# Optimization experiments

Measured on AMD Instinct MI355X. Metric: run time of the kernel, lower is better.

Reference implementation:

```python
import jax, jax.numpy as jnp
import numpy as np

B, D_IN, H, V, T = 8192, 2048, 1024, 6, 6  # batch, enc input, hidden, total_vocab, max_length
TAU = 1.0

def setup_inputs() -> dict:
    key = jax.random.key(0)
    ks = jax.random.split(key, 16)
    s = 0.02
    return {
        "x": jax.random.normal(ks[0], (B, D_IN), jnp.float32),
        "u_noise": jax.random.uniform(ks[1], (T, B, V), jnp.float32),
        "W_enc": jax.random.normal(ks[2], (D_IN, H), jnp.float32) * s,
        "b_enc": jnp.zeros((H,), jnp.float32),
        "start_embed": jax.random.normal(ks[3], (H,), jnp.float32) * 0.01,
        "W_tok": jax.random.normal(ks[4], (V, H), jnp.float32) * s,
        "b_tok": jnp.zeros((H,), jnp.float32),
        "Wz": jax.random.normal(ks[5], (2 * H, H), jnp.float32) * s,
        "bz": jnp.zeros((H,), jnp.float32),
        "Wr": jax.random.normal(ks[6], (2 * H, H), jnp.float32) * s,
        "br": jnp.zeros((H,), jnp.float32),
        "Wh": jax.random.normal(ks[7], (2 * H, H), jnp.float32) * s,
        "bh": jnp.zeros((H,), jnp.float32),
        "W_out": jax.random.normal(ks[8], (H, V), jnp.float32) * s,
        "b_out": jnp.zeros((V,), jnp.float32),
    }

def reference(x, u_noise, W_enc, b_enc, start_embed, W_tok, b_tok,
              Wz, bz, Wr, br, Wh, bh, W_out, b_out):
    eps = 1e-10
    # uniform -> Gumbel(0,1) noise, precomputed per step: (T, B, V)
    g_all = -jnp.log(-jnp.log(u_noise + eps) + eps)
    h0 = x @ W_enc + b_enc                                   # encoder: (B, H)
    batch = x.shape[0]
    prev0 = jnp.broadcast_to(start_embed, (batch, start_embed.shape[0]))
    rc0 = jnp.ones((batch, 1), x.dtype)                      # running continue mask
    nt0 = jnp.zeros((batch,), x.dtype)                       # differentiable token count

    def step(carry, g):
        h, prev, rc, nt = carry
        nt = nt + rc[:, 0]
        comb = jnp.concatenate([prev, h], axis=-1)           # (B, 2H)
        z = jax.nn.sigmoid(comb @ Wz + bz)
        r = jax.nn.sigmoid(comb @ Wr + br)
        comb_r = jnp.concatenate([prev, r * h], axis=-1)
        h_tilde = jnp.tanh(comb_r @ Wh + bh)
        h = (1 - z) * h + z * h_tilde                        # GRU update
        logits = h @ W_out + b_out                           # (B, V)
        # hard gumbel-softmax with straight-through estimator
        y_soft = jax.nn.softmax((logits + g) / TAU, axis=-1)
        y_hard = jax.nn.one_hot(jnp.argmax(y_soft, axis=-1), logits.shape[-1],
                                dtype=logits.dtype)
        token = y_hard - jax.lax.stop_gradient(y_soft) + y_soft
        masked = token * rc                                  # zero out after STOP
        rc = rc * (1 - token[:, -1:])                        # STOP is last symbol
        prev = token @ W_tok + b_tok
        return (h, prev, rc, nt), (masked, logits)

    (_, _, _, n_tokens), (masked_seq, logits_seq) = jax.lax.scan(
        step, (h0, prev0, rc0, nt0), g_all)
    # (T, B, V) -> (B, T*V) message
    message = jnp.transpose(masked_seq, (1, 0, 2)).reshape(batch, -1)
    return message, logits_seq, n_tokens
```

## Files before the change

kernel.cpp:

```cpp
#include <hip/hip_runtime.h>
#include <math.h>

#define B_ 8192
#define DIN_ 2048
#define H_ 1024
#define V_ 6
#define T_ 6

typedef short bf16x8 __attribute__((ext_vector_type(8)));
typedef float f32x4 __attribute__((ext_vector_type(4)));

__device__ __forceinline__ unsigned short f32_bf16(float f) {
    unsigned u = __float_as_uint(f);
    u += 0x7FFFu + ((u >> 16) & 1u);
    return (unsigned short)(u >> 16);
}
__device__ __forceinline__ float bf16_f32(unsigned short h) {
    return __uint_as_float(((unsigned)h) << 16);
}

#define GLL16(g, l) __builtin_amdgcn_global_load_lds(                       \
        (const __attribute__((address_space(1))) void*)(g),                  \
        (__attribute__((address_space(3))) void*)(l), 16, 0, 0)

__global__ __launch_bounds__(256) void conv_w(const float* __restrict__ W,
        unsigned short* __restrict__ hi, unsigned short* __restrict__ lo)
{
    const int t = blockIdx.x * 256 + threadIdx.x;
    const int n = t & 1023;
    const int kb = t >> 10;
    unsigned hq[4], lq[4];
#pragma unroll
    for (int p = 0; p < 4; ++p) {
        const float v0 = W[(size_t)(kb * 8 + 2 * p) * 1024 + n];
        const float v1 = W[(size_t)(kb * 8 + 2 * p + 1) * 1024 + n];
        const unsigned short h0 = f32_bf16(v0), h1 = f32_bf16(v1);
        const unsigned short l0 = f32_bf16(v0 - bf16_f32(h0));
        const unsigned short l1 = f32_bf16(v1 - bf16_f32(h1));
        hq[p] = (unsigned)h0 | ((unsigned)h1 << 16);
        lq[p] = (unsigned)l0 | ((unsigned)l1 << 16);
    }
    const size_t c = ((size_t)(n >> 4) * 256 + kb) * 128 + (size_t)(n & 15) * 8;
    *(uint4*)(hi + c) = make_uint4(hq[0], hq[1], hq[2], hq[3]);
    *(uint4*)(lo + c) = make_uint4(lq[0], lq[1], lq[2], lq[3]);
}

__global__ __launch_bounds__(256) void conv_wb(const float* __restrict__ W,
        unsigned short* __restrict__ hi, unsigned short* __restrict__ lo)
{
    const int t = blockIdx.x * 256 + threadIdx.x;
    const int n = t & 1023;
    const int kb = t >> 10;
    unsigned hq[4], lq[4];
#pragma unroll
    for (int p = 0; p < 4; ++p) {
        const float v0 = W[(size_t)(1024 + kb * 8 + 2 * p) * 1024 + n];
        const float v1 = W[(size_t)(1024 + kb * 8 + 2 * p + 1) * 1024 + n];
        const unsigned short h0 = f32_bf16(v0), h1 = f32_bf16(v1);
        const unsigned short l0 = f32_bf16(v0 - bf16_f32(h0));
        const unsigned short l1 = f32_bf16(v1 - bf16_f32(h1));
        hq[p] = (unsigned)h0 | ((unsigned)h1 << 16);
        lq[p] = (unsigned)l0 | ((unsigned)l1 << 16);
    }
    const size_t c = ((size_t)(n >> 4) * 128 + kb) * 128 + (size_t)(n & 15) * 8;
    *(uint4*)(hi + c) = make_uint4(hq[0], hq[1], hq[2], hq[3]);
    *(uint4*)(lo + c) = make_uint4(lq[0], lq[1], lq[2], lq[3]);
}

__global__ __launch_bounds__(256) void conv_x(const float* __restrict__ X,
        unsigned short* __restrict__ hi, unsigned short* __restrict__ lo)
{
    const size_t t = (size_t)blockIdx.x * 256 + threadIdx.x;
    const int kb = (int)(t & 255);
    const int m = (int)(t >> 8);
    const float4 f0 = *(const float4*)(X + (size_t)m * 2048 + kb * 8);
    const float4 f1 = *(const float4*)(X + (size_t)m * 2048 + kb * 8 + 4);
    const float v[8] = {f0.x, f0.y, f0.z, f0.w, f1.x, f1.y, f1.z, f1.w};
    unsigned hq[4], lq[4];
#pragma unroll
    for (int p = 0; p < 4; ++p) {
        const unsigned short h0 = f32_bf16(v[2 * p]);
        const unsigned short h1 = f32_bf16(v[2 * p + 1]);
        const unsigned short l0 = f32_bf16(v[2 * p] - bf16_f32(h0));
        const unsigned short l1 = f32_bf16(v[2 * p + 1] - bf16_f32(h1));
        hq[p] = (unsigned)h0 | ((unsigned)h1 << 16);
        lq[p] = (unsigned)l0 | ((unsigned)l1 << 16);
    }
    const size_t c = ((size_t)(m >> 4) * 256 + kb) * 128 + (size_t)(m & 15) * 8;
    *(uint4*)(hi + c) = make_uint4(hq[0], hq[1], hq[2], hq[3]);
    *(uint4*)(lo + c) = make_uint4(lq[0], lq[1], lq[2], lq[3]);
}

__global__ __launch_bounds__(256) void prep_tables(
        const float* __restrict__ Wz, const float* __restrict__ Wr,
        const float* __restrict__ Wh,
        const float* __restrict__ bz, const float* __restrict__ br,
        const float* __restrict__ bh,
        const float* __restrict__ Wt, const float* __restrict__ bt,
        const float* __restrict__ se,
        float* __restrict__ Pz, float* __restrict__ Pr, float* __restrict__ Ph)
{
    __shared__ float emb[7][1024];
    const int tid = threadIdx.x;
    for (int i = tid; i < 7 * 1024; i += 256) {
        const int r = i >> 10, k = i & 1023;
        emb[r][k] = (r < 6) ? (Wt[(size_t)r * 1024 + k] + bt[k]) : se[k];
    }
    __syncthreads();
    const float* W = (blockIdx.y == 0) ? Wz : ((blockIdx.y == 1) ? Wr : Wh);
    const float* bb = (blockIdx.y == 0) ? bz : ((blockIdx.y == 1) ? br : bh);
    float* P = (blockIdx.y == 0) ? Pz : ((blockIdx.y == 1) ? Pr : Ph);
    const int n = blockIdx.x * 256 + tid;
    float acc[7] = {0.f, 0.f, 0.f, 0.f, 0.f, 0.f, 0.f};
    for (int k = 0; k < 1024; ++k) {
        const float wv = W[(size_t)k * 1024 + n];
#pragma unroll
        for (int r = 0; r < 7; ++r) acc[r] = fmaf(emb[r][k], wv, acc[r]);
    }
    const float bvv = bb[n];
#pragma unroll
    for (int r = 0; r < 7; ++r) P[(size_t)r * 1024 + n] = acc[r] + bvv;
}

__global__ __launch_bounds__(256) void init_misc(
        int* __restrict__ tokidx, float* __restrict__ rc, float* __restrict__ nt)
{
    const int t = blockIdx.x * 256 + threadIdx.x;
    tokidx[t] = 6;
    rc[t] = 1.0f;
    nt[t] = 0.0f;
}

__global__ __launch_bounds__(256, 3)
void gemm_bt(
    const unsigned short* __restrict__ A_hi, const unsigned short* __restrict__ A_lo,
    const unsigned short* __restrict__ B0_hi, const unsigned short* __restrict__ B0_lo,
    const unsigned short* __restrict__ B1_hi, const unsigned short* __restrict__ B1_lo,
    const float* __restrict__ P0, const float* __restrict__ P1,
    const int* __restrict__ tokidx,
    const float* __restrict__ zbuf, float* __restrict__ hbuf,
    float* __restrict__ outf,
    unsigned short* __restrict__ ophi, unsigned short* __restrict__ oplo,
    int nkb, int mode)
{
    __shared__ unsigned short lds[16384];

    const int tid = threadIdx.x;
    const int lane = tid & 63;
    const int w = tid >> 6;

    const int NX = gridDim.x;
    const int lin = blockIdx.y * NX + blockIdx.x;
    const int xcd = lin & 7;
    const int idx = lin >> 3;
    int bx = idx % NX;
    const int by = xcd * 8 + idx / NX;

    const unsigned short* Bhi = B0_hi;
    const unsigned short* Blo = B0_lo;
    const float* Pm = P0;
    int isR = 0;
    if (mode == 1 && bx >= 8) { bx -= 8; Bhi = B1_hi; Blo = B1_lo; Pm = P1; isR = 1; }

    const int m0 = by * 128;
    const int n0 = bx * 128;
    const int gma0 = by * 8 + 2 * w;
    const int gnb0 = bx * 8 + 2 * w;

    unsigned short* dA0h = lds + (2 * w) * 512 + lane * 8;
    unsigned short* dA1h = lds + (2 * w + 1) * 512 + lane * 8;
    unsigned short* dA0l = lds + 4096 + (2 * w) * 512 + lane * 8;
    unsigned short* dA1l = lds + 4096 + (2 * w + 1) * 512 + lane * 8;
    unsigned short* dB0h = lds + 8192 + (2 * w) * 512 + lane * 8;
    unsigned short* dB1h = lds + 8192 + (2 * w + 1) * 512 + lane * 8;
    unsigned short* dB0l = lds + 12288 + (2 * w) * 512 + lane * 8;
    unsigned short* dB1l = lds + 12288 + (2 * w + 1) * 512 + lane * 8;

    f32x4 acc[4][4];
#pragma unroll
    for (int i = 0; i < 4; ++i)
#pragma unroll
        for (int j = 0; j < 4; ++j) acc[i][j] = (f32x4){0.f, 0.f, 0.f, 0.f};

    const int wr = w >> 1, wc = w & 1;
    const int fq = lane >> 4;
    const int fm = lane & 15;
    const int nsteps = nkb >> 2;

#pragma unroll 1
    for (int s = 0; s < nsteps; ++s) {
        __syncthreads();
        const size_t o0 = ((size_t)gma0 * nkb + s * 4) * 128 + lane * 8;
        const size_t o1 = o0 + (size_t)nkb * 128;
        GLL16(A_hi + o0, dA0h); GLL16(A_lo + o0, dA0l);
        GLL16(A_hi + o1, dA1h); GLL16(A_lo + o1, dA1l);
        const size_t b0 = ((size_t)gnb0 * nkb + s * 4) * 128 + lane * 8;
        const size_t b1 = b0 + (size_t)nkb * 128;
        GLL16(Bhi + b0, dB0h); GLL16(Blo + b0, dB0l);
        GLL16(Bhi + b1, dB1h); GLL16(Blo + b1, dB1l);
        __syncthreads();

        bf16x8 ah[4], al[4], bh4[4], bl4[4];
#pragma unroll
        for (int i = 0; i < 4; ++i) {
            const int ra = (wr * 4 + i) * 512 + fq * 128 + fm * 8;
            ah[i] = *(const bf16x8*)(lds + ra);
            al[i] = *(const bf16x8*)(lds + 4096 + ra);
            const int rb = (wc * 4 + i) * 512 + fq * 128 + fm * 8;
            bh4[i] = *(const bf16x8*)(lds + 8192 + rb);
            bl4[i] = *(const bf16x8*)(lds + 12288 + rb);
        }
#pragma unroll
        for (int i = 0; i < 4; ++i)
#pragma unroll
            for (int j = 0; j < 4; ++j) {
                acc[i][j] = __builtin_amdgcn_mfma_f32_16x16x32_bf16(ah[i], bh4[j], acc[i][j], 0, 0, 0);
                acc[i][j] = __builtin_amdgcn_mfma_f32_16x16x32_bf16(ah[i], bl4[j], acc[i][j], 0, 0, 0);
                acc[i][j] = __builtin_amdgcn_mfma_f32_16x16x32_bf16(al[i], bh4[j], acc[i][j], 0, 0, 0);
            }
    }

#pragma unroll
    for (int i = 0; i < 4; ++i) {
        int toks[4];
#pragma unroll
        for (int r = 0; r < 4; ++r) {
            const int row = m0 + wr * 64 + i * 16 + fq * 4 + r;
            toks[r] = tokidx ? tokidx[row] : 0;
        }
#pragma unroll
        for (int j = 0; j < 4; ++j) {
            const int col = n0 + wc * 64 + j * 16 + fm;
#pragma unroll
            for (int r = 0; r < 4; ++r) {
                const int row = m0 + wr * 64 + i * 16 + fq * 4 + r;
                const float v = acc[i][j][r] + Pm[(size_t)toks[r] * 1024 + col];
                const size_t off = (size_t)row * 1024 + col;
                const size_t pc = ((size_t)(row >> 4) * 128 + (col >> 3)) * 128
                                  + (size_t)(row & 15) * 8 + (col & 7);
                if (mode == 0) {
                    hbuf[off] = v;
                    const unsigned short hv = f32_bf16(v);
                    ophi[pc] = hv;
                    oplo[pc] = f32_bf16(v - bf16_f32(hv));
                } else if (mode == 1) {
                    const float sg = 1.0f / (1.0f + expf(-v));
                    if (!isR) {
                        outf[off] = sg;
                    } else {
                        const float rh = sg * hbuf[off];
                        const unsigned short hv = f32_bf16(rh);
                        ophi[pc] = hv;
                        oplo[pc] = f32_bf16(rh - bf16_f32(hv));
                    }
                } else {
                    const float tv = tanhf(v);
                    const float zv = zbuf[off];
                    const float hn = (1.0f - zv) * hbuf[off] + zv * tv;
                    hbuf[off] = hn;
                    const unsigned short hv = f32_bf16(hn);
                    ophi[pc] = hv;
                    oplo[pc] = f32_bf16(hn - bf16_f32(hv));
                }
            }
        }
    }
}

__global__ __launch_bounds__(256)
void step_tok(const float* __restrict__ h,
              const float* __restrict__ W_out, const float* __restrict__ b_out,
              const float* __restrict__ u,
              float* __restrict__ rc, float* __restrict__ nt,
              int* __restrict__ tokidx,
              float* __restrict__ out_msg, float* __restrict__ out_logits,
              float* __restrict__ out_nt, int t)
{
    const int lane = threadIdx.x & 63;
    const int wv = threadIdx.x >> 6;
    const int b = blockIdx.x * 4 + wv;

    const float* hr = h + (size_t)b * H_;
    float s[6] = {0.f, 0.f, 0.f, 0.f, 0.f, 0.f};
#pragma unroll
    for (int i = 0; i < 4; ++i) {
        const int k0 = i * 256 + lane * 4;
        const float4 hv = *(const float4*)(hr + k0);
        const float he[4] = {hv.x, hv.y, hv.z, hv.w};
#pragma unroll
        for (int e = 0; e < 4; ++e) {
            const float* wp = W_out + (size_t)(k0 + e) * V_;
            const float xv = he[e];
#pragma unroll
            for (int v = 0; v < 6; ++v) s[v] = fmaf(xv, wp[v], s[v]);
        }
    }
#pragma unroll
    for (int m = 1; m < 64; m <<= 1) {
#pragma unroll
        for (int v = 0; v < 6; ++v) s[v] += __shfl_xor(s[v], m, 64);
    }

    float lg[6];
#pragma unroll
    for (int v = 0; v < 6; ++v) lg[v] = s[v] + b_out[v];

    const float* ub = u + (size_t)b * V_;
    const float eps = 1e-10f;
    float aa[6];
#pragma unroll
    for (int v = 0; v < 6; ++v) {
        const float g = -logf(-logf(ub[v] + eps) + eps);
        aa[v] = lg[v] + g;
    }
    int tok = 0;
    float best = aa[0];
#pragma unroll
    for (int v = 1; v < 6; ++v)
        if (aa[v] > best) { best = aa[v]; tok = v; }

    if (lane == 0) {
        const float rco = rc[b];
#pragma unroll
        for (int v = 0; v < 6; ++v) out_logits[(size_t)b * 6 + v] = lg[v];
#pragma unroll
        for (int v = 0; v < 6; ++v)
            out_msg[(size_t)b * 36 + t * 6 + v] = (v == tok) ? rco : 0.0f;
        const float ntn = nt[b] + rco;
        nt[b] = ntn;
        out_nt[b] = ntn;
        rc[b] = (tok == 5) ? 0.0f : rco;
        tokidx[b] = tok;
    }
}

extern "C" void kernel_launch(void* const* d_in, const int* in_sizes, int n_in,
                              void* d_out, int out_size, void* d_ws, size_t ws_size,
                              hipStream_t stream)
{
    (void)in_sizes; (void)n_in; (void)out_size; (void)ws_size;
    const float* x       = (const float*)d_in[0];
    const float* u_noise = (const float*)d_in[1];
    const float* W_enc   = (const float*)d_in[2];
    const float* b_enc   = (const float*)d_in[3];
    const float* start_e = (const float*)d_in[4];
    const float* W_tok   = (const float*)d_in[5];
    const float* b_tok   = (const float*)d_in[6];
    const float* Wz      = (const float*)d_in[7];
    const float* bz      = (const float*)d_in[8];
    const float* Wr      = (const float*)d_in[9];
    const float* br      = (const float*)d_in[10];
    const float* Wh      = (const float*)d_in[11];
    const float* bh      = (const float*)d_in[12];
    const float* W_out   = (const float*)d_in[13];
    const float* b_out   = (const float*)d_in[14];

    float* out = (float*)d_out;
    float* out_msg = out;
    float* out_logits = out + (size_t)B_ * T_ * V_;
    float* out_nt = out_logits + (size_t)T_ * B_ * V_;

    char* wsb = (char*)d_ws;
    const size_t MB = 1024 * 1024;
    unsigned short* wzb_hi = (unsigned short*)(wsb + 0 * MB);
    unsigned short* wzb_lo = (unsigned short*)(wsb + 2 * MB);
    unsigned short* wrb_hi = (unsigned short*)(wsb + 4 * MB);
    unsigned short* wrb_lo = (unsigned short*)(wsb + 6 * MB);
    unsigned short* whb_hi = (unsigned short*)(wsb + 8 * MB);
    unsigned short* whb_lo = (unsigned short*)(wsb + 10 * MB);
    unsigned short* we_hi  = (unsigned short*)(wsb + 12 * MB);
    unsigned short* we_lo  = (unsigned short*)(wsb + 16 * MB);
    unsigned short* x_hi   = (unsigned short*)(wsb + 20 * MB);
    unsigned short* x_lo   = (unsigned short*)(wsb + 52 * MB);
    float*  zbuf  = (float*)(wsb + 20 * MB);
    unsigned short* rh_hi  = (unsigned short*)(wsb + 52 * MB);
    unsigned short* rh_lo  = (unsigned short*)(wsb + 68 * MB);
    float*  hbuf  = (float*)(wsb + 84 * MB);
    unsigned short* h_hi   = (unsigned short*)(wsb + 116 * MB);
    unsigned short* h_lo   = (unsigned short*)(wsb + 132 * MB);
    float* Pz = (float*)(wsb + 148 * MB);
    float* Pr = Pz + 7 * 1024;
    float* Ph = Pr + 7 * 1024;
    int* tokidx = (int*)(Ph + 7 * 1024);
    float* rcb = (float*)(tokidx + B_);
    float* ntb = rcb + B_;

    conv_wb<<<512, 256, 0, stream>>>(Wz, wzb_hi, wzb_lo);
    conv_wb<<<512, 256, 0, stream>>>(Wr, wrb_hi, wrb_lo);
    conv_wb<<<512, 256, 0, stream>>>(Wh, whb_hi, whb_lo);
    conv_w<<<1024, 256, 0, stream>>>(W_enc, we_hi, we_lo);
    conv_x<<<8192, 256, 0, stream>>>(x, x_hi, x_lo);
    prep_tables<<<dim3(4, 3), 256, 0, stream>>>(Wz, Wr, Wh, bz, br, bh,
                                                W_tok, b_tok, start_e, Pz, Pr, Ph);
    init_misc<<<32, 256, 0, stream>>>(tokidx, rcb, ntb);

    gemm_bt<<<dim3(8, 64), 256, 0, stream>>>(
        x_hi, x_lo, we_hi, we_lo, nullptr, nullptr,
        b_enc, nullptr, nullptr,
        nullptr, hbuf, nullptr, h_hi, h_lo, 256, 0);

    for (int t = 0; t < T_; ++t) {
        gemm_bt<<<dim3(16, 64), 256, 0, stream>>>(
            h_hi, h_lo, wzb_hi, wzb_lo, wrb_hi, wrb_lo,
            Pz, Pr, tokidx,
            nullptr, hbuf, zbuf, rh_hi, rh_lo, 128, 1);
        gemm_bt<<<dim3(8, 64), 256, 0, stream>>>(
            rh_hi, rh_lo, whb_hi, whb_lo, nullptr, nullptr,
            Ph, nullptr, tokidx,
            zbuf, hbuf, nullptr, h_hi, h_lo, 128, 2);
        step_tok<<<B_ / 4, 256, 0, stream>>>(
            hbuf, W_out, b_out, u_noise + (size_t)t * B_ * V_,
            rcb, ntb, tokidx, out_msg,
            out_logits + (size_t)t * B_ * V_, out_nt, t);
    }
}
```

Measured before the change: 1.746 ms.

## Rewrite GEMM as 256x128 tile, 512 threads, triple-buffered LDS pipeline

Widens the GEMM block to 512 threads covering 256 rows by 128 columns and splits the hi/lo loading across wave halves. Adds a three-stage LDS ring buffer with direct global-to-LDS prefetch two steps ahead, explicit vmcnt waits, raw barriers and MFMA priority hints. This is meant to hide global load latency behind MFMA work and raise reuse of B tiles. In exchange it uses much more LDS per block (144KB), which lowers occupancy, and the hand-tuned waitcnt counts could be wrong.

New measurement: 1.876 ms. 1.07x slower.

```diff
diff --git a/kernel.cpp b/kernel.cpp
--- a/kernel.cpp
+++ b/kernel.cpp
@@ -131,8 +131,8 @@
     nt[t] = 0.0f;
 }
 
-__global__ __launch_bounds__(256, 3)
-void gemm_bt(
+__global__ __launch_bounds__(512, 2)
+void gemm256(
     const unsigned short* __restrict__ A_hi, const unsigned short* __restrict__ A_lo,
     const unsigned short* __restrict__ B0_hi, const unsigned short* __restrict__ B0_lo,
     const unsigned short* __restrict__ B1_hi, const unsigned short* __restrict__ B1_lo,
@@ -143,7 +143,7 @@
     unsigned short* __restrict__ ophi, unsigned short* __restrict__ oplo,
     int nkb, int mode)
 {
-    __shared__ unsigned short lds[16384];
+    __shared__ unsigned short lds[3 * 24576];
 
     const int tid = threadIdx.x;
     const int lane = tid & 63;
@@ -154,7 +154,7 @@
     const int xcd = lin & 7;
     const int idx = lin >> 3;
     int bx = idx % NX;
-    const int by = xcd * 8 + idx / NX;
+    const int by = xcd * 4 + idx / NX;
 
     const unsigned short* Bhi = B0_hi;
     const unsigned short* Blo = B0_lo;
@@ -162,19 +162,16 @@
     int isR = 0;
     if (mode == 1 && bx >= 8) { bx -= 8; Bhi = B1_hi; Blo = B1_lo; Pm = P1; isR = 1; }
 
-    const int m0 = by * 128;
+    const int m0 = by * 256;
     const int n0 = bx * 128;
-    const int gma0 = by * 8 + 2 * w;
-    const int gnb0 = bx * 8 + 2 * w;
-
-    unsigned short* dA0h = lds + (2 * w) * 512 + lane * 8;
-    unsigned short* dA1h = lds + (2 * w + 1) * 512 + lane * 8;
-    unsigned short* dA0l = lds + 4096 + (2 * w) * 512 + lane * 8;
-    unsigned short* dA1l = lds + 4096 + (2 * w + 1) * 512 + lane * 8;
-    unsigned short* dB0h = lds + 8192 + (2 * w) * 512 + lane * 8;
-    unsigned short* dB1h = lds + 8192 + (2 * w + 1) * 512 + lane * 8;
-    unsigned short* dB0l = lds + 12288 + (2 * w) * 512 + lane * 8;
-    unsigned short* dB1l = lds + 12288 + (2 * w + 1) * 512 + lane * 8;
+    const int mg0 = by * 16;
+    const int ng0 = bx * 8;
+
+    const int pa = w >> 2;
+    const int ga0 = (w & 3) * 4;
+    const int nb0 = (w & 3) * 2;
+    const unsigned short* Asrc = pa ? A_lo : A_hi;
+    const unsigned short* Bsrc = pa ? Blo : Bhi;
 
     f32x4 acc[4][4];
 #pragma unroll
@@ -182,43 +179,84 @@
 #pragma unroll
         for (int j = 0; j < 4; ++j) acc[i][j] = (f32x4){0.f, 0.f, 0.f, 0.f};
 
-    const int wr = w >> 1, wc = w & 1;
+    const int wr = w & 3;
+    const int wc = w >> 2;
     const int fq = lane >> 4;
     const int fm = lane & 15;
     const int nsteps = nkb >> 2;
 
+#define STAGE(tt, bb) do {                                                     \
+    unsigned short* db_ = lds + (bb) * 24576;                                  \
+    const size_t kb0_ = (size_t)(tt) * 4;                                      \
+    _Pragma("unroll")                                                          \
+    for (int q = 0; q < 4; ++q) {                                              \
+        const size_t so = ((size_t)(mg0 + ga0 + q) * nkb + kb0_) * 128 + lane * 8; \
+        GLL16(Asrc + so, db_ + pa * 8192 + (ga0 + q) * 512 + lane * 8);        \
+    }                                                                          \
+    _Pragma("unroll")                                                          \
+    for (int q = 0; q < 2; ++q) {                                              \
+        const size_t so = ((size_t)(ng0 + nb0 + q) * nkb + kb0_) * 128 + lane * 8; \
+        GLL16(Bsrc + so, db_ + 16384 + pa * 4096 + (nb0 + q) * 512 + lane * 8);\
+    }                                                                          \
+} while (0)
+
+#define COMPUTE(bb) do {                                                       \
+    const unsigned short* db_ = lds + (bb) * 24576;                            \
+    bf16x8 bh4_[4], bl4_[4];                                                   \
+    _Pragma("unroll")                                                          \
+    for (int j = 0; j < 4; ++j) {                                              \
+        const int rb = 16384 + (wc * 4 + j) * 512 + fq * 128 + fm * 8;         \
+        bh4_[j] = *(const bf16x8*)(db_ + rb);                                  \
+        bl4_[j] = *(const bf16x8*)(db_ + rb + 4096);                           \
+    }                                                                          \
+    _Pragma("unroll")                                                          \
+    for (int i = 0; i < 4; ++i) {                                              \
+        const int ra = (wr * 4 + i) * 512 + fq * 128 + fm * 8;                 \
+        const bf16x8 ah = *(const bf16x8*)(db_ + ra);                          \
+        const bf16x8 al = *(const bf16x8*)(db_ + ra + 8192);                   \
+        __builtin_amdgcn_s_setprio(1);                                         \
+        _Pragma("unroll")                                                      \
+        for (int j = 0; j < 4; ++j) {                                          \
+            acc[i][j] = __builtin_amdgcn_mfma_f32_16x16x32_bf16(ah, bh4_[j], acc[i][j], 0, 0, 0); \
+            acc[i][j] = __builtin_amdgcn_mfma_f32_16x16x32_bf16(ah, bl4_[j], acc[i][j], 0, 0, 0); \
+            acc[i][j] = __builtin_amdgcn_mfma_f32_16x16x32_bf16(al, bh4_[j], acc[i][j], 0, 0, 0); \
+        }                                                                      \
+        __builtin_amdgcn_s_setprio(0);                                         \
+    }                                                                          \
+} while (0)
+
+    STAGE(0, 0);
+    STAGE(1, 1);
+
+    int cb = 0;
 #pragma unroll 1
-    for (int s = 0; s < nsteps; ++s) {
-        __syncthreads();
-        const size_t o0 = ((size_t)gma0 * nkb + s * 4) * 128 + lane * 8;
-        const size_t o1 = o0 + (size_t)nkb * 128;
-        GLL16(A_hi + o0, dA0h); GLL16(A_lo + o0, dA0l);
-        GLL16(A_hi + o1, dA1h); GLL16(A_lo + o1, dA1l);
-        const size_t b0 = ((size_t)gnb0 * nkb + s * 4) * 128 + lane * 8;
-        const size_t b1 = b0 + (size_t)nkb * 128;
-        GLL16(Bhi + b0, dB0h); GLL16(Blo + b0, dB0l);
-        GLL16(Bhi + b1, dB1h); GLL16(Blo + b1, dB1l);
-        __syncthreads();
-
-        bf16x8 ah[4], al[4], bh4[4], bl4[4];
-#pragma unroll
-        for (int i = 0; i < 4; ++i) {
-            const int ra = (wr * 4 + i) * 512 + fq * 128 + fm * 8;
-            ah[i] = *(const bf16x8*)(lds + ra);
-            al[i] = *(const bf16x8*)(lds + 4096 + ra);
-            const int rb = (wc * 4 + i) * 512 + fq * 128 + fm * 8;
-            bh4[i] = *(const bf16x8*)(lds + 8192 + rb);
-            bl4[i] = *(const bf16x8*)(lds + 12288 + rb);
-        }
-#pragma unroll
-        for (int i = 0; i < 4; ++i)
-#pragma unroll
-            for (int j = 0; j < 4; ++j) {
-                acc[i][j] = __builtin_amdgcn_mfma_f32_16x16x32_bf16(ah[i], bh4[j], acc[i][j], 0, 0, 0);
-                acc[i][j] = __builtin_amdgcn_mfma_f32_16x16x32_bf16(ah[i], bl4[j], acc[i][j], 0, 0, 0);
-                acc[i][j] = __builtin_amdgcn_mfma_f32_16x16x32_bf16(al[i], bh4[j], acc[i][j], 0, 0, 0);
-            }
-    }
+    for (int t = 0; t < nsteps - 2; ++t) {
+        const int sb = (cb >= 1) ? (cb - 1) : 2;
+        STAGE(t + 2, sb);
+        asm volatile("s_waitcnt vmcnt(12)" ::: "memory");
+        __builtin_amdgcn_s_barrier();
+        __builtin_amdgcn_sched_barrier(0);
+        COMPUTE(cb);
+        asm volatile("s_waitcnt lgkmcnt(0)" ::: "memory");
+        __builtin_amdgcn_s_barrier();
+        __builtin_amdgcn_sched_barrier(0);
+        cb = (cb == 2) ? 0 : cb + 1;
+    }
+    asm volatile("s_waitcnt vmcnt(6)" ::: "memory");
+    __builtin_amdgcn_s_barrier();
+    __builtin_amdgcn_sched_barrier(0);
+    COMPUTE(cb);
+    asm volatile("s_waitcnt lgkmcnt(0)" ::: "memory");
+    __builtin_amdgcn_s_barrier();
+    __builtin_amdgcn_sched_barrier(0);
+    cb = (cb == 2) ? 0 : cb + 1;
+    asm volatile("s_waitcnt vmcnt(0)" ::: "memory");
+    __builtin_amdgcn_s_barrier();
+    __builtin_amdgcn_sched_barrier(0);
+    COMPUTE(cb);
+
+#undef STAGE
+#undef COMPUTE
 
 #pragma unroll
     for (int i = 0; i < 4; ++i) {
@@ -394,17 +432,17 @@
                                                 W_tok, b_tok, start_e, Pz, Pr, Ph);
     init_misc<<<32, 256, 0, stream>>>(tokidx, rcb, ntb);
 
-    gemm_bt<<<dim3(8, 64), 256, 0, stream>>>(
+    gemm256<<<dim3(8, 32), 512, 0, stream>>>(
         x_hi, x_lo, we_hi, we_lo, nullptr, nullptr,
         b_enc, nullptr, nullptr,
         nullptr, hbuf, nullptr, h_hi, h_lo, 256, 0);
 
     for (int t = 0; t < T_; ++t) {
-        gemm_bt<<<dim3(16, 64), 256, 0, stream>>>(
+        gemm256<<<dim3(16, 32), 512, 0, stream>>>(
             h_hi, h_lo, wzb_hi, wzb_lo, wrb_hi, wrb_lo,
             Pz, Pr, tokidx,
             nullptr, hbuf, zbuf, rh_hi, rh_lo, 128, 1);
-        gemm_bt<<<dim3(8, 64), 256, 0, stream>>>(
+        gemm256<<<dim3(8, 32), 512, 0, stream>>>(
             rh_hi, rh_lo, whb_hi, whb_lo, nullptr, nullptr,
             Ph, nullptr, tokidx,
             zbuf, hbuf, nullptr, h_hi, h_lo, 128, 2);
```

## Fuse z and r gate GEMMs into one kernel sharing the A tile

Applied to the files above, without the earlier changes.

Adds a gemm_zr kernel that computes the z and r gate products together for the same 128x128 output tile. Each block loads the h tile once and reuses it against both Wz and Wr, so A traffic is halved and the grid goes from 16x64 to 8x64 blocks. The cost is two accumulator sets per thread, which raises register pressure (launch bounds ask for 2 blocks per CU), and a larger LDS footprint.

Result: slower. 1.904 ms (+9.0%).

```diff
diff --git a/kernel.cpp b/kernel.cpp
--- a/kernel.cpp
+++ b/kernel.cpp
@@ -267,6 +267,133 @@
     }
 }
 
+__global__ __launch_bounds__(256, 2)
+void gemm_zr(
+    const unsigned short* __restrict__ A_hi, const unsigned short* __restrict__ A_lo,
+    const unsigned short* __restrict__ Bz_hi, const unsigned short* __restrict__ Bz_lo,
+    const unsigned short* __restrict__ Br_hi, const unsigned short* __restrict__ Br_lo,
+    const float* __restrict__ Pz, const float* __restrict__ Pr,
+    const int* __restrict__ tokidx,
+    const float* __restrict__ hbuf, float* __restrict__ zbuf,
+    unsigned short* __restrict__ ophi, unsigned short* __restrict__ oplo,
+    int nkb)
+{
+    __shared__ unsigned short lds[24576];
+
+    const int tid = threadIdx.x;
+    const int lane = tid & 63;
+    const int w = tid >> 6;
+
+    const int NX = gridDim.x;
+    const int lin = blockIdx.y * NX + blockIdx.x;
+    const int xcd = lin & 7;
+    const int idx = lin >> 3;
+    const int bx = idx % NX;
+    const int by = xcd * 8 + idx / NX;
+
+    const int m0 = by * 128;
+    const int n0 = bx * 128;
+    const int gma0 = by * 8 + 2 * w;
+    const int gnb0 = bx * 8 + 2 * w;
+
+    unsigned short* dAh0 = lds +         (2 * w) * 512 + lane * 8;
+    unsigned short* dAh1 = lds +         (2 * w + 1) * 512 + lane * 8;
+    unsigned short* dAl0 = lds + 4096 +  (2 * w) * 512 + lane * 8;
+    unsigned short* dAl1 = lds + 4096 +  (2 * w + 1) * 512 + lane * 8;
+    unsigned short* dZh0 = lds + 8192 +  (2 * w) * 512 + lane * 8;
+    unsigned short* dZh1 = lds + 8192 +  (2 * w + 1) * 512 + lane * 8;
+    unsigned short* dZl0 = lds + 12288 + (2 * w) * 512 + lane * 8;
+    unsigned short* dZl1 = lds + 12288 + (2 * w + 1) * 512 + lane * 8;
+    unsigned short* dRh0 = lds + 16384 + (2 * w) * 512 + lane * 8;
+    unsigned short* dRh1 = lds + 16384 + (2 * w + 1) * 512 + lane * 8;
+    unsigned short* dRl0 = lds + 20480 + (2 * w) * 512 + lane * 8;
+    unsigned short* dRl1 = lds + 20480 + (2 * w + 1) * 512 + lane * 8;
+
+    f32x4 accz[4][4], accr[4][4];
+#pragma unroll
+    for (int i = 0; i < 4; ++i)
+#pragma unroll
+        for (int j = 0; j < 4; ++j) {
+            accz[i][j] = (f32x4){0.f, 0.f, 0.f, 0.f};
+            accr[i][j] = (f32x4){0.f, 0.f, 0.f, 0.f};
+        }
+
+    const int wr = w >> 1, wc = w & 1;
+    const int fq = lane >> 4;
+    const int fm = lane & 15;
+    const int nsteps = nkb >> 2;
+
+#pragma unroll 1
+    for (int s = 0; s < nsteps; ++s) {
+        __syncthreads();
+        const size_t a0 = ((size_t)gma0 * nkb + s * 4) * 128 + lane * 8;
+        const size_t a1 = a0 + (size_t)nkb * 128;
+        GLL16(A_hi + a0, dAh0); GLL16(A_lo + a0, dAl0);
+        GLL16(A_hi + a1, dAh1); GLL16(A_lo + a1, dAl1);
+        const size_t b0 = ((size_t)gnb0 * nkb + s * 4) * 128 + lane * 8;
+        const size_t b1 = b0 + (size_t)nkb * 128;
+        GLL16(Bz_hi + b0, dZh0); GLL16(Bz_lo + b0, dZl0);
+        GLL16(Bz_hi + b1, dZh1); GLL16(Bz_lo + b1, dZl1);
+        GLL16(Br_hi + b0, dRh0); GLL16(Br_lo + b0, dRl0);
+        GLL16(Br_hi + b1, dRh1); GLL16(Br_lo + b1, dRl1);
+        __syncthreads();
+
+        bf16x8 ah[4], al[4];
+#pragma unroll
+        for (int i = 0; i < 4; ++i) {
+            const int ra = (wr * 4 + i) * 512 + fq * 128 + fm * 8;
+            ah[i] = *(const bf16x8*)(lds + ra);
+            al[i] = *(const bf16x8*)(lds + 4096 + ra);
+        }
+#pragma unroll
+        for (int j = 0; j < 4; ++j) {
+            const int rb = (wc * 4 + j) * 512 + fq * 128 + fm * 8;
+            const bf16x8 bzh = *(const bf16x8*)(lds + 8192 + rb);
+            const bf16x8 bzl = *(const bf16x8*)(lds + 12288 + rb);
+            const bf16x8 brh = *(const bf16x8*)(lds + 16384 + rb);
+            const bf16x8 brl = *(const bf16x8*)(lds + 20480 + rb);
+#pragma unroll
+            for (int i = 0; i < 4; ++i) {
+                accz[i][j] = __builtin_amdgcn_mfma_f32_16x16x32_bf16(ah[i], bzh, accz[i][j], 0, 0, 0);
+                accz[i][j] = __builtin_amdgcn_mfma_f32_16x16x32_bf16(ah[i], bzl, accz[i][j], 0, 0, 0);
+                accz[i][j] = __builtin_amdgcn_mfma_f32_16x16x32_bf16(al[i], bzh, accz[i][j], 0, 0, 0);
+                accr[i][j] = __builtin_amdgcn_mfma_f32_16x16x32_bf16(ah[i], brh, accr[i][j], 0, 0, 0);
+                accr[i][j] = __builtin_amdgcn_mfma_f32_16x16x32_bf16(ah[i], brl, accr[i][j], 0, 0, 0);
+                accr[i][j] = __builtin_amdgcn_mfma_f32_16x16x32_bf16(al[i], brh, accr[i][j], 0, 0, 0);
+            }
+        }
+    }
+
+#pragma unroll
+    for (int i = 0; i < 4; ++i) {
+        int toks[4];
+#pragma unroll
+        for (int r = 0; r < 4; ++r) {
+            const int row = m0 + wr * 64 + i * 16 + fq * 4 + r;
+            toks[r] = tokidx[row];
+        }
+#pragma unroll
+        for (int j = 0; j < 4; ++j) {
+            const int col = n0 + wc * 64 + j * 16 + fm;
+#pragma unroll
+            for (int r = 0; r < 4; ++r) {
+                const int row = m0 + wr * 64 + i * 16 + fq * 4 + r;
+                const size_t off = (size_t)row * 1024 + col;
+                const size_t pc = ((size_t)(row >> 4) * 128 + (col >> 3)) * 128
+                                  + (size_t)(row & 15) * 8 + (col & 7);
+                const float vz = accz[i][j][r] + Pz[(size_t)toks[r] * 1024 + col];
+                zbuf[off] = 1.0f / (1.0f + expf(-vz));
+                const float vr = accr[i][j][r] + Pr[(size_t)toks[r] * 1024 + col];
+                const float sgr = 1.0f / (1.0f + expf(-vr));
+                const float rh = sgr * hbuf[off];
+                const unsigned short hv = f32_bf16(rh);
+                ophi[pc] = hv;
+                oplo[pc] = f32_bf16(rh - bf16_f32(hv));
+            }
+        }
+    }
+}
+
 __global__ __launch_bounds__(256)
 void step_tok(const float* __restrict__ h,
               const float* __restrict__ W_out, const float* __restrict__ b_out,
@@ -400,10 +527,10 @@
         nullptr, hbuf, nullptr, h_hi, h_lo, 256, 0);
 
     for (int t = 0; t < T_; ++t) {
-        gemm_bt<<<dim3(16, 64), 256, 0, stream>>>(
+        gemm_zr<<<dim3(8, 64), 256, 0, stream>>>(
             h_hi, h_lo, wzb_hi, wzb_lo, wrb_hi, wrb_lo,
             Pz, Pr, tokidx,
-            nullptr, hbuf, zbuf, rh_hi, rh_lo, 128, 1);
+            hbuf, zbuf, rh_hi, rh_lo, 128);
         gemm_bt<<<dim3(8, 64), 256, 0, stream>>>(
             rh_hi, rh_lo, whb_hi, whb_lo, nullptr, nullptr,
             Ph, nullptr, tokidx,
```
